# Kernel tuning notes

Measured on AMD Instinct MI355X. Metric: run time of the kernel, lower is better.

## Reference

```python
import jax, jax.numpy as jnp
import numpy as np

C = 64
CQ = C // 4
G = 8  # group norm groups
EPS_GN = 1e-5
POS_COEF = 0.1


def setup_inputs() -> dict:
    key = jax.random.key(0)
    ks = jax.random.split(key, 12)
    B, N = 2, 4096
    return {
        "context_features": jax.random.normal(ks[0], (B, C, N), jnp.float32),
        "motion_features": jax.random.normal(ks[1], (B, C, N), jnp.float32),
        "xyz1": jax.random.uniform(ks[2], (B, N, 3), jnp.float32),
        # tied q/k conv weight (Conv1d k=1, no bias): (C//4, C)
        "Wqk": jax.random.normal(ks[3], (CQ, C), jnp.float32) * 0.1,
        # v_conv: Conv1d(C, C, 1) with bias
        "Wv": jax.random.normal(ks[4], (C, C), jnp.float32) * 0.1,
        "bv": jax.random.normal(ks[5], (C,), jnp.float32) * 0.1,
        # trans_conv: Conv1d(C, C, 1) with bias
        "Wt": jax.random.normal(ks[6], (C, C), jnp.float32) * 0.1,
        "bt": jax.random.normal(ks[7], (C,), jnp.float32) * 0.1,
        # GroupNorm(8, C) affine params
        "gn_w": jax.random.normal(ks[8], (C,), jnp.float32) * 0.1 + 1.0,
        "gn_b": jax.random.normal(ks[9], (C,), jnp.float32) * 0.1,
        # PReLU single slope, alpha_gma scalar (init 0 in torch; random here for testing)
        "prelu_a": jnp.float32(0.25) + jax.random.normal(ks[10], (), jnp.float32) * 0.01,
        "alpha": jax.random.normal(ks[11], (), jnp.float32) * 0.1,
    }


def _group_norm(x, w, b):
    # x: (B, C, N)
    B, Cc, N = x.shape
    xg = x.reshape(B, G, Cc // G, N)
    mu = xg.mean(axis=(2, 3), keepdims=True)
    var = xg.var(axis=(2, 3), keepdims=True)
    xn = ((xg - mu) * jax.lax.rsqrt(var + EPS_GN)).reshape(B, Cc, N)
    return xn * w[None, :, None] + b[None, :, None]


def reference(context_features, motion_features, xyz1, Wqk, Wv, bv, Wt, bt, gn_w, gn_b, prelu_a, alpha):
    # --- self attention (tied q/k) ---
    q = jnp.einsum("oc,bcn->bon", Wqk, context_features)  # (B, C/4, N)
    corr = jnp.einsum("bom,bon->bmn", q, q)               # (B, N, N)
    attn = jax.nn.softmax(corr, axis=-1)
    attn = attn / (1e-9 + attn.sum(axis=1, keepdims=True))

    # --- position mask via Gram-trick squared distances ---
    sq = jnp.sum(xyz1 * xyz1, axis=-1)                    # (B, N)
    d = sq[:, :, None] + sq[:, None, :] - 2.0 * jnp.einsum("bid,bjd->bij", xyz1, xyz1)
    d = jnp.maximum(d, 0.0)
    pos_am = d / (1e-9 + d.sum(axis=1, keepdims=True))
    mask = pos_am <= POS_COEF

    local = attn * mask
    local = jax.nn.softmax(local, axis=-1)
    local = local / (1e-9 + local.sum(axis=1, keepdims=True))
    attn = attn + local

    # --- GMA fusion ---
    xv = jnp.einsum("oc,bcn->bon", Wv, motion_features) + bv[None, :, None]
    gma = jnp.einsum("bcm,bmn->bcn", xv, attn)
    res = jnp.einsum("oc,bcn->bon", Wt, motion_features - gma) + bt[None, :, None]
    gr = _group_norm(res, gn_w, gn_b)
    gr = jnp.where(gr >= 0, gr, prelu_a * gr)  # PReLU
    return alpha * gr + motion_features
```

## Files before the change

### kernel.cpp

```cpp
#include <hip/hip_runtime.h>
#include <hip/hip_bf16.h>
#include <cstdio>

#define NB 2
#define NN 4096
#define NC 64
#define NQ 16
#define POS_COEF 0.1f

#define OFF_QT   0u
#define OFF_QK   131072u
#define OFF_XYZ4 262144u
#define OFF_XYZK 294912u
#define OFF_IRS1 327680u
#define OFF_IRS2 335872u
#define OFF_THR  344064u
#define OFF_ICS1 352256u
#define OFF_FLAG 360448u
#define OFF_XVB  360464u
#define OFF_SUMS 622608u
#define OFF_GN   622616u
#define OFF_CS2  622648u
#define OFF_GMA  630840u
#define OFF_G2   1155128u
#define WS_TOTAL 1679416u
#define ZERO_F   (WS_TOTAL - OFF_SUMS)
#define OFF_A0   1679424u
#define OFF_AE   18456640u
#define FULL_F   35233856u

using bf16x8 = __attribute__((ext_vector_type(8))) short;
using f32x4v = __attribute__((ext_vector_type(4))) float;

__device__ __forceinline__ float rcpf_(float x) { return __builtin_amdgcn_rcpf(x); }
__device__ __forceinline__ unsigned short f2bf(float x) {
  __hip_bfloat16 h = __float2bfloat16(x);
  return *(unsigned short*)&h;
}
__device__ __forceinline__ float bf2f(unsigned short u) {
  unsigned v = ((unsigned)u) << 16;
  return __builtin_bit_cast(float, v);
}

__device__ __forceinline__ float ldin(const void* p, size_t i, bool f32) {
  return f32 ? ((const float*)p)[i]
             : __bfloat162float(((const __hip_bfloat16*)p)[i]);
}

#define DOT16M(A0,A1,A2,A3,B0,B1,B2,B3) \
  fmaf((A0).x,(B0).x, fmaf((A0).y,(B0).y, fmaf((A0).z,(B0).z, fmaf((A0).w,(B0).w, \
  fmaf((A1).x,(B1).x, fmaf((A1).y,(B1).y, fmaf((A1).z,(B1).z, fmaf((A1).w,(B1).w, \
  fmaf((A2).x,(B2).x, fmaf((A2).y,(B2).y, fmaf((A2).z,(B2).z, fmaf((A2).w,(B2).w, \
  fmaf((A3).x,(B3).x, fmaf((A3).y,(B3).y, fmaf((A3).z,(B3).z, (A3).w*(B3).w)))))))))))))))

#define DOTC(M0,M1,M2,M3,C) \
  fmaf((M0).x,k0.C, fmaf((M0).y,k1.C, fmaf((M0).z,k2.C, fmaf((M0).w,k3.C, \
  fmaf((M1).x,k4.C, fmaf((M1).y,k5.C, fmaf((M1).z,k6.C, fmaf((M1).w,k7.C, \
  fmaf((M2).x,k8.C, fmaf((M2).y,k9.C, fmaf((M2).z,k10.C, fmaf((M2).w,k11.C, \
  fmaf((M3).x,k12.C, fmaf((M3).y,k13.C, fmaf((M3).z,k14.C, (M3).w*k15.C)))))))))))))))

#define LKPL(base, n0) \
  const float4 k0  = *(const float4*)((base) + 0*NN  + (n0)); \
  const float4 k1  = *(const float4*)((base) + 1*NN  + (n0)); \
  const float4 k2  = *(const float4*)((base) + 2*NN  + (n0)); \
  const float4 k3  = *(const float4*)((base) + 3*NN  + (n0)); \
  const float4 k4  = *(const float4*)((base) + 4*NN  + (n0)); \
  const float4 k5  = *(const float4*)((base) + 5*NN  + (n0)); \
  const float4 k6  = *(const float4*)((base) + 6*NN  + (n0)); \
  const float4 k7  = *(const float4*)((base) + 7*NN  + (n0)); \
  const float4 k8  = *(const float4*)((base) + 8*NN  + (n0)); \
  const float4 k9  = *(const float4*)((base) + 9*NN  + (n0)); \
  const float4 k10 = *(const float4*)((base) + 10*NN + (n0)); \
  const float4 k11 = *(const float4*)((base) + 11*NN + (n0)); \
  const float4 k12 = *(const float4*)((base) + 12*NN + (n0)); \
  const float4 k13 = *(const float4*)((base) + 13*NN + (n0)); \
  const float4 k14 = *(const float4*)((base) + 14*NN + (n0)); \
  const float4 k15 = *(const float4*)((base) + 15*NN + (n0));

#define WRED(s) { s += __shfl_xor(s, 32); s += __shfl_xor(s, 16); \
  s += __shfl_xor(s, 8); s += __shfl_xor(s, 4); s += __shfl_xor(s, 2); s += __shfl_xor(s, 1); }

#define LQROW(v, base) \
  const float4 v##0 = *(const float4*)((base)); \
  const float4 v##1 = *(const float4*)((base) + 4); \
  const float4 v##2 = *(const float4*)((base) + 8); \
  const float4 v##3 = *(const float4*)((base) + 12);

__global__ __launch_bounds__(256) void k0_detect(
    const unsigned short* __restrict__ ctx_u16, float* __restrict__ flag) {
  const int tid = threadIdx.x;
  int bad = 0;
  for (int i = tid; i < 8192; i += 256) {
    const unsigned short u = ctx_u16[i];
    const int e = (u >> 7) & 0xFF;
    if (e >= 134 || (e >= 1 && e <= 100)) bad++;
  }
  __shared__ int cnt;
  if (tid == 0) cnt = 0;
  __syncthreads();
  atomicAdd(&cnt, bad);
  __syncthreads();
  if (tid == 0) flag[0] = (cnt > 256) ? 1.0f : 0.0f;
}

__global__ __launch_bounds__(256) void k1_q_xyz(
    const void* __restrict__ ctx, const void* __restrict__ xyz,
    const void* __restrict__ wqk, const float* __restrict__ flag,
    float* __restrict__ qt, float* __restrict__ qk,
    float* __restrict__ xyz4, float* __restrict__ xyzk,
    float* __restrict__ sums) {
  const bool f32 = flag[0] > 0.5f;
  const int tid = threadIdx.x;
  const int b = blockIdx.x >> 4;
  const int n = ((blockIdx.x & 15) << 8) + tid;
  __shared__ float wqT[NQ * NC];
  for (int i = tid; i < NQ * NC; i += 256) {
    int o = i & 15, c = i >> 4;
    wqT[c * 16 + o] = ldin(wqk, o * 64 + c, f32);
  }
  __syncthreads();
  float4 a0 = {0,0,0,0}, a1 = {0,0,0,0}, a2 = {0,0,0,0}, a3 = {0,0,0,0};
  const size_t cbase = (size_t)b * 64 * NN + n;
#pragma unroll 4
  for (int c = 0; c < 64; ++c) {
    float x = ldin(ctx, cbase + (size_t)c * NN, f32);
    const float4 w0 = *(const float4*)(wqT + c * 16 + 0);
    const float4 w1 = *(const float4*)(wqT + c * 16 + 4);
    const float4 w2 = *(const float4*)(wqT + c * 16 + 8);
    const float4 w3 = *(const float4*)(wqT + c * 16 + 12);
// ... 312 lines not shown
  LQROW(mb, qb + (size_t)mB * 16)
  float sA = 0.f, sB = 0.f;
  for (int it = 0; it < 8; ++it) {
    const int n0 = (it << 9) + (lane << 3);
    float4 aAl = {0,0,0,0}, aAh = {0,0,0,0}, aBl = {0,0,0,0}, aBh = {0,0,0,0};
#define PLN(QA_, QB_, P) { \
      const float4 kl_ = *(const float4*)(kb + (size_t)(P) * NN + n0); \
      const float4 kh_ = *(const float4*)(kb + (size_t)(P) * NN + n0 + 4); \
      aAl.x = fmaf(QA_, kl_.x, aAl.x); aAl.y = fmaf(QA_, kl_.y, aAl.y); \
      aAl.z = fmaf(QA_, kl_.z, aAl.z); aAl.w = fmaf(QA_, kl_.w, aAl.w); \
      aAh.x = fmaf(QA_, kh_.x, aAh.x); aAh.y = fmaf(QA_, kh_.y, aAh.y); \
      aAh.z = fmaf(QA_, kh_.z, aAh.z); aAh.w = fmaf(QA_, kh_.w, aAh.w); \
      aBl.x = fmaf(QB_, kl_.x, aBl.x); aBl.y = fmaf(QB_, kl_.y, aBl.y); \
      aBl.z = fmaf(QB_, kl_.z, aBl.z); aBl.w = fmaf(QB_, kl_.w, aBl.w); \
      aBh.x = fmaf(QB_, kh_.x, aBh.x); aBh.y = fmaf(QB_, kh_.y, aBh.y); \
      aBh.z = fmaf(QB_, kh_.z, aBh.z); aBh.w = fmaf(QB_, kh_.w, aBh.w); }
    PLN(ma0.x, mb0.x, 0)   PLN(ma0.y, mb0.y, 1)
    PLN(ma0.z, mb0.z, 2)   PLN(ma0.w, mb0.w, 3)
    PLN(ma1.x, mb1.x, 4)   PLN(ma1.y, mb1.y, 5)
    PLN(ma1.z, mb1.z, 6)   PLN(ma1.w, mb1.w, 7)
    PLN(ma2.x, mb2.x, 8)   PLN(ma2.y, mb2.y, 9)
    PLN(ma2.z, mb2.z, 10)  PLN(ma2.w, mb2.w, 11)
    PLN(ma3.x, mb3.x, 12)  PLN(ma3.y, mb3.y, 13)
    PLN(ma3.z, mb3.z, 14)  PLN(ma3.w, mb3.w, 15)
#undef PLN
#define EX8(AL, AH, S, ROWPTR) { \
      const unsigned short u0_ = f2bf(__expf(fminf((AL).x, 80.f))); \
      const unsigned short u1_ = f2bf(__expf(fminf((AL).y, 80.f))); \
      const unsigned short u2_ = f2bf(__expf(fminf((AL).z, 80.f))); \
      const unsigned short u3_ = f2bf(__expf(fminf((AL).w, 80.f))); \
      const unsigned short u4_ = f2bf(__expf(fminf((AH).x, 80.f))); \
      const unsigned short u5_ = f2bf(__expf(fminf((AH).y, 80.f))); \
      const unsigned short u6_ = f2bf(__expf(fminf((AH).z, 80.f))); \
      const unsigned short u7_ = f2bf(__expf(fminf((AH).w, 80.f))); \
      uint4 U_; \
      U_.x = (unsigned)u0_ | ((unsigned)u1_ << 16); \
      U_.y = (unsigned)u2_ | ((unsigned)u3_ << 16); \
      U_.z = (unsigned)u4_ | ((unsigned)u5_ << 16); \
      U_.w = (unsigned)u6_ | ((unsigned)u7_ << 16); \
      *(uint4*)((ROWPTR) + n0) = U_; \
      S += bf2f(u0_) + bf2f(u1_) + bf2f(u2_) + bf2f(u3_) \
         + bf2f(u4_) + bf2f(u5_) + bf2f(u6_) + bf2f(u7_); }
    EX8(aAl, aAh, sA, ab + (size_t)mA * NN)
    EX8(aBl, aBh, sB, ab + (size_t)mB * NN)
#undef EX8
  }
  WRED(sA) WRED(sB)
  if (lane == 0) {
    irs1[b * NN + mA] = rcpf_(sA);
    irs1[b * NN + mB] = rcpf_(sB);
  }
}

__global__ __launch_bounds__(256) void p2r_cs1(
    const unsigned short* __restrict__ a0g, const float* __restrict__ irs1,
    float* __restrict__ ics1) {
  const int tid = threadIdx.x;
  const int w = tid >> 6, l = tid & 63;
  const int bi = blockIdx.x;
  const int b = bi >> 10;
  const int n = ((bi & 1023) << 2) + w;
  const unsigned short* row = a0g + ((size_t)b * NN + n) * NN;
  const float* ir = irs1 + b * NN;
  float s = 0.f;
#pragma unroll
  for (int it = 0; it < 8; ++it) {
    const int m = (it << 9) + (l << 3);
    const uint4 u = *(const uint4*)(row + m);
    const float4 i0 = *(const float4*)(ir + m);
    const float4 i1 = *(const float4*)(ir + m + 4);
    s = fmaf(bf2f((unsigned short)(u.x & 0xffffu)), i0.x, s);
    s = fmaf(bf2f((unsigned short)(u.x >> 16)),     i0.y, s);
    s = fmaf(bf2f((unsigned short)(u.y & 0xffffu)), i0.z, s);
    s = fmaf(bf2f((unsigned short)(u.y >> 16)),     i0.w, s);
    s = fmaf(bf2f((unsigned short)(u.z & 0xffffu)), i1.x, s);
    s = fmaf(bf2f((unsigned short)(u.z >> 16)),     i1.y, s);
    s = fmaf(bf2f((unsigned short)(u.w & 0xffffu)), i1.z, s);
    s = fmaf(bf2f((unsigned short)(u.w >> 16)),     i1.w, s);
  }
  WRED(s)
  if (l == 0) ics1[b * NN + n] = rcpf_(1e-9f + s);
}

__global__ __launch_bounds__(256) void p3w_rs2(
    const float* __restrict__ xyz4, const float* __restrict__ xyzk,
    const float* __restrict__ irs1, const float* __restrict__ ics1,
    const float* __restrict__ thr, float* __restrict__ irs2,
    const unsigned short* __restrict__ a0g, unsigned short* __restrict__ aeg) {
  const int tid = threadIdx.x;
  const int b = blockIdx.x >> 9;
  const int m0 = (blockIdx.x & 511) << 3;
  const int w = tid >> 6, lane = tid & 63;
  const float* xk = xyzk + (size_t)b * 4 * NN;
  const unsigned short* ab = a0g + (size_t)b * NN * NN;
  unsigned short* eb = aeg + (size_t)b * NN * NN;
  const int mA = m0 + (w << 1), mB = mA + 1;
  const float4 pmA = *(const float4*)(xyz4 + ((size_t)b * NN + mA) * 4);
  const float4 pmB = *(const float4*)(xyz4 + ((size_t)b * NN + mB) * 4);
  const float rA = irs1[b * NN + mA];
  const float rB = irs1[b * NN + mB];
  float sA = 0.f, sB = 0.f;
#define P3E(S, OUT, A0W, SH, PM, R, PX, PY, PZ, PW, IC, TH) { \
    float a1v_ = bf2f((unsigned short)(((A0W) >> (SH)) & 0xffffu)) * (R) * (IC); \
    float dd_ = (PM).w + (PW) - 2.f * ((PM).x * (PX) + (PM).y * (PY) + (PM).z * (PZ)); \
    dd_ = fmaxf(dd_, 0.f); \
    float l0_ = (dd_ <= (TH)) ? a1v_ : 0.f; \
    const unsigned short us_ = f2bf(__expf(l0_)); OUT = us_; S += bf2f(us_); }
  for (int it = 0; it < 8; ++it) {
    const int n0 = (it << 9) + (lane << 3);
    const float4 pxl = *(const float4*)(xk + 0*NN + n0);
    const float4 pxh = *(const float4*)(xk + 0*NN + n0 + 4);
    const float4 pyl = *(const float4*)(xk + 1*NN + n0);
    const float4 pyh = *(const float4*)(xk + 1*NN + n0 + 4);
    const float4 pzl = *(const float4*)(xk + 2*NN + n0);
    const float4 pzh = *(const float4*)(xk + 2*NN + n0 + 4);
    const float4 pwl = *(const float4*)(xk + 3*NN + n0);
    const float4 pwh = *(const float4*)(xk + 3*NN + n0 + 4);
    const float4 icl = *(const float4*)(ics1 + b * NN + n0);
    const float4 ich = *(const float4*)(ics1 + b * NN + n0 + 4);
    const float4 thl = *(const float4*)(thr + b * NN + n0);
    const float4 thh = *(const float4*)(thr + b * NN + n0 + 4);
    const uint4 rAu = *(const uint4*)(ab + (size_t)mA * NN + n0);
    const uint4 rBu = *(const uint4*)(ab + (size_t)mB * NN + n0);
    unsigned short e0, e1, e2, e3, e4, e5, e6, e7;
    P3E(sA, e0, rAu.x, 0,  pmA, rA, pxl.x, pyl.x, pzl.x, pwl.x, icl.x, thl.x)
    P3E(sA, e1, rAu.x, 16, pmA, rA, pxl.y, pyl.y, pzl.y, pwl.y, icl.y, thl.y)
    P3E(sA, e2, rAu.y, 0,  pmA, rA, pxl.z, pyl.z, pzl.z, pwl.z, icl.z, thl.z)
    P3E(sA, e3, rAu.y, 16, pmA, rA, pxl.w, pyl.w, pzl.w, pwl.w, icl.w, thl.w)
    P3E(sA, e4, rAu.z, 0,  pmA, rA, pxh.x, pyh.x, pzh.x, pwh.x, ich.x, thh.x)
    P3E(sA, e5, rAu.z, 16, pmA, rA, pxh.y, pyh.y, pzh.y, pwh.y, ich.y, thh.y)
    P3E(sA, e6, rAu.w, 0,  pmA, rA, pxh.z, pyh.z, pzh.z, pwh.z, ich.z, thh.z)
    P3E(sA, e7, rAu.w, 16, pmA, rA, pxh.w, pyh.w, pzh.w, pwh.w, ich.w, thh.w)
    {
      uint4 U_;
      U_.x = (unsigned)e0 | ((unsigned)e1 << 16);
      U_.y = (unsigned)e2 | ((unsigned)e3 << 16);
      U_.z = (unsigned)e4 | ((unsigned)e5 << 16);
      U_.w = (unsigned)e6 | ((unsigned)e7 << 16);
      *(uint4*)(eb + (size_t)mA * NN + n0) = U_;
    }
    P3E(sB, e0, rBu.x, 0,  pmB, rB, pxl.x, pyl.x, pzl.x, pwl.x, icl.x, thl.x)
    P3E(sB, e1, rBu.x, 16, pmB, rB, pxl.y, pyl.y, pzl.y, pwl.y, icl.y, thl.y)
    P3E(sB, e2, rBu.y, 0,  pmB, rB, pxl.z, pyl.z, pzl.z, pwl.z, icl.z, thl.z)
    P3E(sB, e3, rBu.y, 16, pmB, rB, pxl.w, pyl.w, pzl.w, pwl.w, icl.w, thl.w)
    P3E(sB, e4, rBu.z, 0,  pmB, rB, pxh.x, pyh.x, pzh.x, pwh.x, ich.x, thh.x)
    P3E(sB, e5, rBu.z, 16, pmB, rB, pxh.y, pyh.y, pzh.y, pwh.y, ich.y, thh.y)
    P3E(sB, e6, rBu.w, 0,  pmB, rB, pxh.z, pyh.z, pzh.z, pwh.z, ich.z, thh.z)
    P3E(sB, e7, rBu.w, 16, pmB, rB, pxh.w, pyh.w, pzh.w, pwh.w, ich.w, thh.w)
    {
      uint4 U_;
      U_.x = (unsigned)e0 | ((unsigned)e1 << 16);
      U_.y = (unsigned)e2 | ((unsigned)e3 << 16);
      U_.z = (unsigned)e4 | ((unsigned)e5 << 16);
      U_.w = (unsigned)e6 | ((unsigned)e7 << 16);
      *(uint4*)(eb + (size_t)mB * NN + n0) = U_;
    }
  }
#undef P3E
  WRED(sA) WRED(sB)
  if (lane == 0) {
    irs2[b * NN + mA] = rcpf_(sA);
    irs2[b * NN + mB] = rcpf_(sB);
  }
}

__global__ __launch_bounds__(256) void p4_cs2(
    const unsigned short* __restrict__ aeg, const float* __restrict__ irs2,
    float* __restrict__ cs2) {
  const int tid = threadIdx.x;
  const int bid = blockIdx.x;
  const int ms = bid & 63;
  const int ng = (bid >> 6) & 7;
  const int b  = bid >> 9;
  const int n2 = (ng << 9) + (tid << 1);
  const unsigned short* eb = aeg + (size_t)b * NN * NN + n2;
  const float* r2 = irs2 + b * NN;
  float s0 = 0.f, s1 = 0.f;
  const int m0 = ms << 6;
#pragma unroll 4
  for (int m = m0; m < m0 + 64; ++m) {
    const unsigned u = *(const unsigned*)(eb + (size_t)m * NN);
    const float r = r2[m];
    s0 += bf2f(f2bf(bf2f((unsigned short)(u & 0xffffu)) * r));
    s1 += bf2f(f2bf(bf2f((unsigned short)(u >> 16)) * r));
  }
  atomicAdd(&cs2[b * NN + n2], s0);
  atomicAdd(&cs2[b * NN + n2 + 1], s1);
}

#define SW(r) ((((r) & 7) << 4) ^ ((((r) >> 3) & 3) << 5))

__global__ __launch_bounds__(256) void k7n_gma(
    const unsigned short* __restrict__ a0g, const unsigned short* __restrict__ aeg,
    const unsigned short* __restrict__ xvb,
    const float* __restrict__ irs1, const float* __restrict__ irs2,
    const float* __restrict__ ics1, const float* __restrict__ cs2,
    float* __restrict__ gma) {
  const int tid = threadIdx.x;
  const int bid = blockIdx.x;
  const int msl = bid & 3;
  const int nb  = (bid >> 2) & 63;
  const int b   = bid >> 8;
  const int n0 = nb << 6;
  const int mstart = msl << 10;
  __shared__ __align__(16) unsigned short attns1[2][64 * 64];
  __shared__ __align__(16) unsigned short attns2[2][64 * 64];
  __shared__ __align__(16) unsigned short xvs[2][64 * 64];
  const unsigned short* ab = a0g + (size_t)b * NN * NN;
  const unsigned short* ebp = aeg + (size_t)b * NN * NN;
  const float* irs1b = irs1 + b * NN;
  const float* irs2b = irs2 + b * NN;
  const int w = tid >> 6, l = tid & 63;
  const int lrow0 = (w << 4) + ((l >> 3) << 1);
  const int nc8 = (l & 7) << 3;
  const int gcol = n0 + nc8;
  const int xc = tid >> 2, xpart = tid & 3;
  const unsigned short* xvp = xvb + ((size_t)b * 64 + xc) * NN;
  const int lr = l & 15, quad = l >> 4;
  const int nw = w << 4;
  f32x4v acc0 = {0,0,0,0}, acc1 = {0,0,0,0}, acc2 = {0,0,0,0}, acc3 = {0,0,0,0};
  f32x4v d0 = {0,0,0,0}, d1 = {0,0,0,0}, d2 = {0,0,0,0}, d3 = {0,0,0,0};

  uint4 pa0A, pa1A, pe0A, pe1A, pv0A, pv1A;
  uint4 pa0B, pa1B, pe0B, pe1B, pv0B, pv1B;
  float r1aA, r1bA, r2aA, r2bA, r1aB, r1bB, r2aB, r2bB;

#define ISSUE(S, MT) { \
    const int m0_ = mstart + ((MT) << 6); \
    const size_t ra_ = (size_t)(m0_ + lrow0) * NN + gcol; \
    pa0##S = *(const uint4*)(ab + ra_); \
    pa1##S = *(const uint4*)(ab + ra_ + NN); \
    pe0##S = *(const uint4*)(ebp + ra_); \
    pe1##S = *(const uint4*)(ebp + ra_ + NN); \
    pv0##S = *(const uint4*)(xvp + m0_ + (xpart << 4)); \
    pv1##S = *(const uint4*)(xvp + m0_ + (xpart << 4) + 8); \
    r1a##S = irs1b[m0_ + lrow0]; r1b##S = irs1b[m0_ + lrow0 + 1]; \
    r2a##S = irs2b[m0_ + lrow0]; r2b##S = irs2b[m0_ + lrow0 + 1]; }

#define CVW(D0, D1, SH, J, R0, R1, ARR) { \
    const float v0_ = bf2f((unsigned short)(((D0) >> (SH)) & 0xffffu)) * (R0); \
    const float v1_ = bf2f((unsigned short)(((D1) >> (SH)) & 0xffffu)) * (R1); \
    const unsigned pk_ = (unsigned)f2bf(v0_) | ((unsigned)f2bf(v1_) << 16); \
    const int nl_ = nc8 + (J); \
    *(unsigned*)((char*)(ARR) + ((((nl_) << 7) + (lrow0 << 1)) ^ SW(nl_))) = pk_; }

#define WR8(U0, U1, R0, R1, ARR) \
    CVW(U0.x, U1.x, 0,  0, R0, R1, ARR) CVW(U0.x, U1.x, 16, 1, R0, R1, ARR) \
    CVW(U0.y, U1.y, 0,  2, R0, R1, ARR) CVW(U0.y, U1.y, 16, 3, R0, R1, ARR) \
    CVW(U0.z, U1.z, 0,  4, R0, R1, ARR) CVW(U0.z, U1.z, 16, 5, R0, R1, ARR) \
    CVW(U0.w, U1.w, 0,  6, R0, R1, ARR) CVW(U0.w, U1.w, 16, 7, R0, R1, ARR)

#define STX(XARR, PV0, PV1) { \
    const int xb_ = (xc << 7) + (xpart << 5); \
    *(uint4*)((char*)(XARR) + ((xb_) ^ SW(xc))) = PV0; \
    *(uint4*)((char*)(XARR) + ((xb_ + 16) ^ SW(xc))) = PV1; }

#define LDSW(ARR, ROW, H, Q) \
    (*(const bf16x8*)((const char*)(ARR) + \
      ((((ROW) << 7) + ((H) << 6) + ((Q) << 4)) ^ SW(ROW))))

#define MPH(A1P, A2P, XVP_) { \
    for (int h = 0; h < 2; ++h) { \
      const bf16x8 fa1 = LDSW(A1P, nw + lr, h, quad); \
      const bf16x8 fa2 = LDSW(A2P, nw + lr, h, quad); \
      const bf16x8 fb0 = LDSW(XVP_, lr, h, quad); \
      const bf16x8 fb1 = LDSW(XVP_, 16 + lr, h, quad); \
      const bf16x8 fb2 = LDSW(XVP_, 32 + lr, h, quad); \
      const bf16x8 fb3 = LDSW(XVP_, 48 + lr, h, quad); \
      acc0 = __builtin_amdgcn_mfma_f32_16x16x32_bf16(fa1, fb0, acc0, 0, 0, 0); \
      acc1 = __builtin_amdgcn_mfma_f32_16x16x32_bf16(fa1, fb1, acc1, 0, 0, 0); \
      acc2 = __builtin_amdgcn_mfma_f32_16x16x32_bf16(fa1, fb2, acc2, 0, 0, 0); \
      acc3 = __builtin_amdgcn_mfma_f32_16x16x32_bf16(fa1, fb3, acc3, 0, 0, 0); \
      d0 = __builtin_amdgcn_mfma_f32_16x16x32_bf16(fa2, fb0, d0, 0, 0, 0); \
      d1 = __builtin_amdgcn_mfma_f32_16x16x32_bf16(fa2, fb1, d1, 0, 0, 0); \
      d2 = __builtin_amdgcn_mfma_f32_16x16x32_bf16(fa2, fb2, d2, 0, 0, 0); \
      d3 = __builtin_amdgcn_mfma_f32_16x16x32_bf16(fa2, fb3, d3, 0, 0, 0); \
    } }

  ISSUE(A, 0)
  ISSUE(B, 1)
  for (int mt = 0; mt < 16; mt += 2) {
    WR8(pa0A, pa1A, r1aA, r1bA, attns1[0])
    WR8(pe0A, pe1A, r2aA, r2bA, attns2[0])
    STX(xvs[0], pv0A, pv1A)
    __syncthreads();
    if (mt + 2 < 16) { ISSUE(A, mt + 2) }
    MPH(attns1[0], attns2[0], xvs[0])
    WR8(pa0B, pa1B, r1aB, r1bB, attns1[1])
    WR8(pe0B, pe1B, r2aB, r2bB, attns2[1])
    STX(xvs[1], pv0B, pv1B)
    __syncthreads();
    if (mt + 3 < 16) { ISSUE(B, mt + 3) }
    MPH(attns1[1], attns2[1], xvs[1])
  }
#undef ISSUE
#undef CVW
#undef WR8
#undef STX
#undef LDSW
#undef MPH
  float w10, w11, w12, w13, w20, w21, w22, w23;
  {
    const int nr = n0 + nw + (quad << 2);
    w10 = ics1[b * NN + nr + 0]; w20 = rcpf_(1e-9f + cs2[b * NN + nr + 0]);
    w11 = ics1[b * NN + nr + 1]; w21 = rcpf_(1e-9f + cs2[b * NN + nr + 1]);
    w12 = ics1[b * NN + nr + 2]; w22 = rcpf_(1e-9f + cs2[b * NN + nr + 2]);
    w13 = ics1[b * NN + nr + 3]; w23 = rcpf_(1e-9f + cs2[b * NN + nr + 3]);
  }
#define EPI(ACC, DD, CT) { \
    float* g_ = gma + ((size_t)b * NN + n0 + nw + (quad << 2)) * 64 + (CT) * 16 + lr; \
    atomicAdd(g_ + 0,   fmaf(ACC[0], w10, DD[0] * w20)); \
    atomicAdd(g_ + 64,  fmaf(ACC[1], w11, DD[1] * w21)); \
    atomicAdd(g_ + 128, fmaf(ACC[2], w12, DD[2] * w22)); \
    atomicAdd(g_ + 192, fmaf(ACC[3], w13, DD[3] * w23)); }
  EPI(acc0, d0, 0) EPI(acc1, d1, 1) EPI(acc2, d2, 2) EPI(acc3, d3, 3)
#undef EPI
}


__global__ __launch_bounds__(256) void p2_cs1(
    const float* __restrict__ qt, const float* __restrict__ qk,
    const float* __restrict__ irs1, float* __restrict__ ics1) {
  const int tid = threadIdx.x;
  const int b = blockIdx.x >> 8;
  const int n0t = (blockIdx.x & 255) << 4;
  const int w = tid >> 6, lane = tid & 63;
  const float* qb = qt + (size_t)b * NN * 16;
  const float* kb = qk + (size_t)b * 16 * NN;
  const int nA = n0t + w, nB = n0t + w + 4, nC = n0t + w + 8, nD = n0t + w + 12;
  LQROW(na, qb + (size_t)nA * 16)
  LQROW(nb, qb + (size_t)nB * 16)
  LQROW(nc, qb + (size_t)nC * 16)
  LQROW(nd, qb + (size_t)nD * 16)
  float sA = 0.f, sB = 0.f, sC = 0.f, sD = 0.f;
  for (int it = 0; it < 16; ++it) {
    const int m0 = (it << 8) + (lane << 2);
    LKPL(kb, m0)
    const float4 r1 = *(const float4*)(irs1 + b * NN + m0);
    sA = fmaf(__expf(fminf(DOTC(na0,na1,na2,na3,x), 80.f)), r1.x, sA);
    sA = fmaf(__expf(fminf(DOTC(na0,na1,na2,na3,y), 80.f)), r1.y, sA);
    sA = fmaf(__expf(fminf(DOTC(na0,na1,na2,na3,z), 80.f)), r1.z, sA);
    sA = fmaf(__expf(fminf(DOTC(na0,na1,na2,na3,w), 80.f)), r1.w, sA);
    sB = fmaf(__expf(fminf(DOTC(nb0,nb1,nb2,nb3,x), 80.f)), r1.x, sB);
    sB = fmaf(__expf(fminf(DOTC(nb0,nb1,nb2,nb3,y), 80.f)), r1.y, sB);
    sB = fmaf(__expf(fminf(DOTC(nb0,nb1,nb2,nb3,z), 80.f)), r1.z, sB);
    sB = fmaf(__expf(fminf(DOTC(nb0,nb1,nb2,nb3,w), 80.f)), r1.w, sB);
    sC = fmaf(__expf(fminf(DOTC(nc0,nc1,nc2,nc3,x), 80.f)), r1.x, sC);
    sC = fmaf(__expf(fminf(DOTC(nc0,nc1,nc2,nc3,y), 80.f)), r1.y, sC);
    sC = fmaf(__expf(fminf(DOTC(nc0,nc1,nc2,nc3,z), 80.f)), r1.z, sC);
    sC = fmaf(__expf(fminf(DOTC(nc0,nc1,nc2,nc3,w), 80.f)), r1.w, sC);
    sD = fmaf(__expf(fminf(DOTC(nd0,nd1,nd2,nd3,x), 80.f)), r1.x, sD);
    sD = fmaf(__expf(fminf(DOTC(nd0,nd1,nd2,nd3,y), 80.f)), r1.y, sD);
    sD = fmaf(__expf(fminf(DOTC(nd0,nd1,nd2,nd3,z), 80.f)), r1.z, sD);
    sD = fmaf(__expf(fminf(DOTC(nd0,nd1,nd2,nd3,w), 80.f)), r1.w, sD);
  }
  WRED(sA) WRED(sB) WRED(sC) WRED(sD)
  if (lane == 0) {
    ics1[b * NN + nA] = rcpf_(1e-9f + sA);
    ics1[b * NN + nB] = rcpf_(1e-9f + sB);
    ics1[b * NN + nC] = rcpf_(1e-9f + sC);
    ics1[b * NN + nD] = rcpf_(1e-9f + sD);
  }
}

__global__ __launch_bounds__(256) void k8_res(
    const void* __restrict__ mot, const void* __restrict__ wt,
    const void* __restrict__ bt, const float* __restrict__ flag,
    float* __restrict__ g1_res, const float* __restrict__ g2,
    const float* __restrict__ cs2, float* __restrict__ gn,
    const float* __restrict__ ics1, int g1mode) {
  const bool f32 = flag[0] > 0.5f;
  const int tid = threadIdx.x;
// ... 7 lines not shown
  for (int i = tid; i < 4096; i += 256) {
    int o = i & 63, c = i >> 6;
    wtT[c * 65 + o] = ldin(wt, o * 64 + c, f32);
  }
  if (tid < 64) bts[tid] = ldin(bt, tid, f32);
  if (tid < 8) { gs[tid] = 0.f; gss[tid] = 0.f; }
#pragma unroll
  for (int r = 0; r < 2; ++r) {
    const int idx = tid * 2 + r;
    const int c = idx & 63, nl = idx >> 6;
    const size_t gi = ((size_t)b * NN + n0 + nl) * 64 + c;
    float gmav;
    if (g1mode == 2) {
      gmav = g1_res[gi];
    } else {
      const float ics2n = rcpf_(1e-9f + cs2[b * NN + n0 + nl]);
      float g1v = g1_res[gi];
      if (g1mode == 1) g1v *= ics1[b * NN + n0 + nl];
      gmav = fmaf(g2[gi], ics2n, g1v);
    }
    md[nl * 64 + c] = ldin(mot, ((size_t)b * 64 + c) * NN + n0 + nl, f32) - gmav;
  }
  __syncthreads();
  const int o = tid & 63, ng = tid >> 6;
  const int nl0 = ng * 2, nl1 = ng * 2 + 1;
  float a0 = bts[o], a1 = bts[o];
#pragma unroll 8
  for (int c = 0; c < 64; ++c) {
    float w = wtT[c * 65 + o];
    a0 = fmaf(w, md[nl0 * 64 + c], a0);
    a1 = fmaf(w, md[nl1 * 64 + c], a1);
  }
  g1_res[((size_t)b * NN + n0 + nl0) * 64 + o] = a0;
  g1_res[((size_t)b * NN + n0 + nl1) * 64 + o] = a1;
  atomicAdd(&gs[o >> 3], a0 + a1);
  atomicAdd(&gss[o >> 3], a0 * a0 + a1 * a1);
  __syncthreads();
  if (tid < 8) atomicAdd(&gn[b * 8 + tid], gs[tid]);
  else if (tid < 16) atomicAdd(&gn[16 + b * 8 + (tid - 8)], gss[tid - 8]);
}

__global__ __launch_bounds__(256) void k9_out(
    const float* __restrict__ res, const float* __restrict__ gn,
    const void* __restrict__ mot,
    const void* __restrict__ gnw, const void* __restrict__ gnb,
    const void* __restrict__ pa, const void* __restrict__ al,
    const float* __restrict__ flag, void* __restrict__ out) {
  const bool f32 = flag[0] > 0.5f;
  const int idx = blockIdx.x * 256 + threadIdx.x;
  const int n = idx & 4095;
  const int c = (idx >> 12) & 63;
  const int b = idx >> 18;
  const int g = c >> 3;
  const float inv_cnt = 1.f / 32768.f;
  float mean = gn[b * 8 + g] * inv_cnt;
  float var = gn[16 + b * 8 + g] * inv_cnt - mean * mean;
  var = fmaxf(var, 0.f);
  float rstd = rsqrtf(var + 1e-5f);
  float r = res[((size_t)b * NN + n) * 64 + c];
  float y = (r - mean) * rstd * ldin(gnw, c, f32) + ldin(gnb, c, f32);
  float slope = ldin(pa, 0, f32);
  y = (y >= 0.f) ? y : slope * y;
  float o = ldin(al, 0, f32) * y + ldin(mot, idx, f32);
  if (f32) ((float*)out)[idx] = o;
  else     ((__hip_bfloat16*)out)[idx] = __float2bfloat16(o);
}

extern "C" void kernel_launch(void* const* d_in, const int* in_sizes, int n_in,
                              void* d_out, int out_size, void* d_ws, size_t ws_size,
                              hipStream_t stream) {
  const void* ctx = d_in[0];
  const void* mot = d_in[1];
  const void* xyz = d_in[2];
  const void* wqk = d_in[3];
  const void* wv  = d_in[4];
  const void* bv  = d_in[5];
  const void* wt  = d_in[6];
  const void* bt  = d_in[7];
  const void* gnw = d_in[8];
  const void* gnb = d_in[9];
  const void* pa  = d_in[10];
  const void* al  = d_in[11];
  float* ws = (float*)d_ws;
  const bool big = ws_size >= (size_t)FULL_F * sizeof(float);

  if (ws_size < (size_t)WS_TOTAL * sizeof(float))
    fprintf(stderr, "[gma3d] WARNING ws_size=%zu < needed %zu\n",
            ws_size, (size_t)WS_TOTAL * sizeof(float));

  hipMemsetAsync(ws + OFF_SUMS, 0, (size_t)ZERO_F * sizeof(float), stream);

  k0_detect<<<1, 256, 0, stream>>>((const unsigned short*)ctx, ws + OFF_FLAG);
  k1_q_xyz<<<32, 256, 0, stream>>>(ctx, xyz, wqk, ws + OFF_FLAG,
                                   ws + OFF_QT, ws + OFF_QK,
                                   ws + OFF_XYZ4, ws + OFF_XYZK, ws + OFF_SUMS);
  k2_xv<<<128, 256, 0, stream>>>(mot, wv, bv, ws + OFF_FLAG,
                                 (unsigned short*)(ws + OFF_XVB));
  k2b_thr<<<32, 256, 0, stream>>>(ws + OFF_XYZ4, ws + OFF_SUMS, ws + OFF_THR);

  if (big) {
    unsigned short* a0 = (unsigned short*)(ws + OFF_A0);
    unsigned short* ae = (unsigned short*)(ws + OFF_AE);
    p1w_rs1<<<1024, 256, 0, stream>>>(ws + OFF_QT, ws + OFF_QK, ws + OFF_IRS1, a0);
    p2r_cs1<<<2048, 256, 0, stream>>>(a0, ws + OFF_IRS1, ws + OFF_ICS1);
    p3w_rs2<<<1024, 256, 0, stream>>>(ws + OFF_XYZ4, ws + OFF_XYZK,
                                      ws + OFF_IRS1, ws + OFF_ICS1, ws + OFF_THR,
                                      ws + OFF_IRS2, a0, ae);
    p4_cs2<<<1024, 256, 0, stream>>>(ae, ws + OFF_IRS2, ws + OFF_CS2);
    k7n_gma<<<512, 256, 0, stream>>>(a0, ae,
                                     (const unsigned short*)(ws + OFF_XVB),
                                     ws + OFF_IRS1, ws + OFF_IRS2,
                                     ws + OFF_ICS1, ws + OFF_CS2,
                                     ws + OFF_GMA);
    k8_res<<<1024, 256, 0, stream>>>(mot, wt, bt, ws + OFF_FLAG,
                                     ws + OFF_GMA, ws + OFF_G2, ws + OFF_CS2,
                                     ws + OFF_GN, ws + OFF_ICS1, 2);
  } else {
    p1_rs1<<<512, 256, 0, stream>>>(ws + OFF_QT, ws + OFF_QK, ws + OFF_IRS1);
    p2_cs1<<<512, 256, 0, stream>>>(ws + OFF_QT, ws + OFF_QK, ws + OFF_IRS1, ws + OFF_ICS1);
    p3_rs2<<<512, 256, 0, stream>>>(ws + OFF_QT, ws + OFF_QK,
                                    ws + OFF_XYZ4, ws + OFF_XYZK,
                                    ws + OFF_IRS1, ws + OFF_ICS1, ws + OFF_THR,
                                    ws + OFF_IRS2);
    k7_gma<<<1024, 256, 0, stream>>>(ws + OFF_QT, ws + OFF_XYZ4,
                                     (const unsigned short*)(ws + OFF_XVB),
                                     ws + OFF_IRS1, ws + OFF_IRS2,
                                     ws + OFF_ICS1, ws + OFF_THR,
                                     ws + OFF_GMA, ws + OFF_G2, ws + OFF_CS2);
    k8_res<<<1024, 256, 0, stream>>>(mot, wt, bt, ws + OFF_FLAG,
                                     ws + OFF_GMA, ws + OFF_G2, ws + OFF_CS2,
                                     ws + OFF_GN, ws + OFF_ICS1, 0);
  }

  k9_out<<<2048, 256, 0, stream>>>(ws + OFF_GMA, ws + OFF_GN, mot, gnw, gnb, pa, al,
                                   ws + OFF_FLAG, d_out);
}
```

Before: 284.3 us.

## Recompute masked local-attention exp values instead of materializing the ae matrix

The pass that computed the masked exp matrix no longer writes a second full N×N bf16 buffer. Each downstream consumer (row-sum pass, column-sum pass, GMA matmul) rebuilds those values from the stored base attention, the xyz positions and the thresholds through a shared helper. This removes one large global write and two large reads, and lowers the workspace needed to enable the precomputed path. In exchange every consumer does extra exp and distance arithmetic, and needs extra position and threshold loads and registers.

```diff
diff --git a/kernel.cpp b/kernel.cpp
--- a/kernel.cpp
+++ b/kernel.cpp
@@ -26,8 +26,7 @@
 #define WS_TOTAL 1679416u
 #define ZERO_F   (WS_TOTAL - OFF_SUMS)
 #define OFF_A0   1679424u
-#define OFF_AE   18456640u
-#define FULL_F   35233856u
+#define BIG_F    18456640u
 
 using bf16x8 = __attribute__((ext_vector_type(8))) short;
 using f32x4v = __attribute__((ext_vector_type(4))) float;
@@ -45,6 +44,16 @@
 __device__ __forceinline__ float ldin(const void* p, size_t i, bool f32) {
   return f32 ? ((const float*)p)[i]
              : __bfloat162float(((const __hip_bfloat16*)p)[i]);
+}
+
+__device__ __forceinline__ unsigned short ae_bits(
+    unsigned short a0u, float r1, float ic, float4 pm,
+    float px, float py, float pz, float pw, float th) {
+  float a1v = bf2f(a0u) * r1 * ic;
+  float dd = pm.w + pw - 2.f * (pm.x * px + pm.y * py + pm.z * pz);
+  dd = fmaxf(dd, 0.f);
+  float l0 = (dd <= th) ? a1v : 0.f;
+  return f2bf(__expf(l0));
 }
 
 #define DOT16M(A0,A1,A2,A3,B0,B1,B2,B3) \
@@ -523,30 +532,23 @@
   if (l == 0) ics1[b * NN + n] = rcpf_(1e-9f + s);
 }
 
-__global__ __launch_bounds__(256) void p3w_rs2(
+__global__ __launch_bounds__(256) void p3r_rs2(
     const float* __restrict__ xyz4, const float* __restrict__ xyzk,
     const float* __restrict__ irs1, const float* __restrict__ ics1,
     const float* __restrict__ thr, float* __restrict__ irs2,
-    const unsigned short* __restrict__ a0g, unsigned short* __restrict__ aeg) {
+    const unsigned short* __restrict__ a0g) {
   const int tid = threadIdx.x;
   const int b = blockIdx.x >> 9;
   const int m0 = (blockIdx.x & 511) << 3;
   const int w = tid >> 6, lane = tid & 63;
   const float* xk = xyzk + (size_t)b * 4 * NN;
   const unsigned short* ab = a0g + (size_t)b * NN * NN;
-  unsigned short* eb = aeg + (size_t)b * NN * NN;
   const int mA = m0 + (w << 1), mB = mA + 1;
   const float4 pmA = *(const float4*)(xyz4 + ((size_t)b * NN + mA) * 4);
   const float4 pmB = *(const float4*)(xyz4 + ((size_t)b * NN + mB) * 4);
   const float rA = irs1[b * NN + mA];
   const float rB = irs1[b * NN + mB];
   float sA = 0.f, sB = 0.f;
-#define P3E(S, OUT, A0W, SH, PM, R, PX, PY, PZ, PW, IC, TH) { \
-    float a1v_ = bf2f((unsigned short)(((A0W) >> (SH)) & 0xffffu)) * (R) * (IC); \
-    float dd_ = (PM).w + (PW) - 2.f * ((PM).x * (PX) + (PM).y * (PY) + (PM).z * (PZ)); \
-    dd_ = fmaxf(dd_, 0.f); \
-    float l0_ = (dd_ <= (TH)) ? a1v_ : 0.f; \
-    const unsigned short us_ = f2bf(__expf(l0_)); OUT = us_; S += bf2f(us_); }
   for (int it = 0; it < 8; ++it) {
     const int n0 = (it << 9) + (lane << 3);
     const float4 pxl = *(const float4*)(xk + 0*NN + n0);
@@ -563,41 +565,27 @@
     const float4 thh = *(const float4*)(thr + b * NN + n0 + 4);
     const uint4 rAu = *(const uint4*)(ab + (size_t)mA * NN + n0);
     const uint4 rBu = *(const uint4*)(ab + (size_t)mB * NN + n0);
-    unsigned short e0, e1, e2, e3, e4, e5, e6, e7;
-    P3E(sA, e0, rAu.x, 0,  pmA, rA, pxl.x, pyl.x, pzl.x, pwl.x, icl.x, thl.x)
-    P3E(sA, e1, rAu.x, 16, pmA, rA, pxl.y, pyl.y, pzl.y, pwl.y, icl.y, thl.y)
-    P3E(sA, e2, rAu.y, 0,  pmA, rA, pxl.z, pyl.z, pzl.z, pwl.z, icl.z, thl.z)
-    P3E(sA, e3, rAu.y, 16, pmA, rA, pxl.w, pyl.w, pzl.w, pwl.w, icl.w, thl.w)
-    P3E(sA, e4, rAu.z, 0,  pmA, rA, pxh.x, pyh.x, pzh.x, pwh.x, ich.x, thh.x)
-    P3E(sA, e5, rAu.z, 16, pmA, rA, pxh.y, pyh.y, pzh.y, pwh.y, ich.y, thh.y)
-    P3E(sA, e6, rAu.w, 0,  pmA, rA, pxh.z, pyh.z, pzh.z, pwh.z, ich.z, thh.z)
-    P3E(sA, e7, rAu.w, 16, pmA, rA, pxh.w, pyh.w, pzh.w, pwh.w, ich.w, thh.w)
-    {
-      uint4 U_;
-      U_.x = (unsigned)e0 | ((unsigned)e1 << 16);
-      U_.y = (unsigned)e2 | ((unsigned)e3 << 16);
-      U_.z = (unsigned)e4 | ((unsigned)e5 << 16);
-      U_.w = (unsigned)e6 | ((unsigned)e7 << 16);
-      *(uint4*)(eb + (size_t)mA * NN + n0) = U_;
-    }
-    P3E(sB, e0, rBu.x, 0,  pmB, rB, pxl.x, pyl.x, pzl.x, pwl.x, icl.x, thl.x)
-    P3E(sB, e1, rBu.x, 16, pmB, rB, pxl.y, pyl.y, pzl.y, pwl.y, icl.y, thl.y)
-    P3E(sB, e2, rBu.y, 0,  pmB, rB, pxl.z, pyl.z, pzl.z, pwl.z, icl.z, thl.z)
-    P3E(sB, e3, rBu.y, 16, pmB, rB, pxl.w, pyl.w, pzl.w, pwl.w, icl.w, thl.w)
-    P3E(sB, e4, rBu.z, 0,  pmB, rB, pxh.x, pyh.x, pzh.x, pwh.x, ich.x, thh.x)
-    P3E(sB, e5, rBu.z, 16, pmB, rB, pxh.y, pyh.y, pzh.y, pwh.y, ich.y, thh.y)
-    P3E(sB, e6, rBu.w, 0,  pmB, rB, pxh.z, pyh.z, pzh.z, pwh.z, ich.z, thh.z)
-    P3E(sB, e7, rBu.w, 16, pmB, rB, pxh.w, pyh.w, pzh.w, pwh.w, ich.w, thh.w)
-    {
-      uint4 U_;
-      U_.x = (unsigned)e0 | ((unsigned)e1 << 16);
-      U_.y = (unsigned)e2 | ((unsigned)e3 << 16);
-      U_.z = (unsigned)e4 | ((unsigned)e5 << 16);
-      U_.w = (unsigned)e6 | ((unsigned)e7 << 16);
-      *(uint4*)(eb + (size_t)mB * NN + n0) = U_;
-    }
-  }
-#undef P3E
+#define P3R1(S, A0W, SH, PM, R, PX, PY, PZ, PW, IC, TH) \
+    S += bf2f(ae_bits((unsigned short)(((A0W) >> (SH)) & 0xffffu), (R), (IC), \
+                      (PM), (PX), (PY), (PZ), (PW), (TH)));
+    P3R1(sA, rAu.x, 0,  pmA, rA, pxl.x, pyl.x, pzl.x, pwl.x, icl.x, thl.x)
+    P3R1(sA, rAu.x, 16, pmA, rA, pxl.y, pyl.y, pzl.y, pwl.y, icl.y, thl.y)
+    P3R1(sA, rAu.y, 0,  pmA, rA, pxl.z, pyl.z, pzl.z, pwl.z, icl.z, thl.z)
+    P3R1(sA, rAu.y, 16, pmA, rA, pxl.w, pyl.w, pzl.w, pwl.w, icl.w, thl.w)
+    P3R1(sA, rAu.z, 0,  pmA, rA, pxh.x, pyh.x, pzh.x, pwh.x, ich.x, thh.x)
+    P3R1(sA, rAu.z, 16, pmA, rA, pxh.y, pyh.y, pzh.y, pwh.y, ich.y, thh.y)
+    P3R1(sA, rAu.w, 0,  pmA, rA, pxh.z, pyh.z, pzh.z, pwh.z, ich.z, thh.z)
+    P3R1(sA, rAu.w, 16, pmA, rA, pxh.w, pyh.w, pzh.w, pwh.w, ich.w, thh.w)
+    P3R1(sB, rBu.x, 0,  pmB, rB, pxl.x, pyl.x, pzl.x, pwl.x, icl.x, thl.x)
+    P3R1(sB, rBu.x, 16, pmB, rB, pxl.y, pyl.y, pzl.y, pwl.y, icl.y, thl.y)
+    P3R1(sB, rBu.y, 0,  pmB, rB, pxl.z, pyl.z, pzl.z, pwl.z, icl.z, thl.z)
+    P3R1(sB, rBu.y, 16, pmB, rB, pxl.w, pyl.w, pzl.w, pwl.w, icl.w, thl.w)
+    P3R1(sB, rBu.z, 0,  pmB, rB, pxh.x, pyh.x, pzh.x, pwh.x, ich.x, thh.x)
+    P3R1(sB, rBu.z, 16, pmB, rB, pxh.y, pyh.y, pzh.y, pwh.y, ich.y, thh.y)
+    P3R1(sB, rBu.w, 0,  pmB, rB, pxh.z, pyh.z, pzh.z, pwh.z, ich.z, thh.z)
+    P3R1(sB, rBu.w, 16, pmB, rB, pxh.w, pyh.w, pzh.w, pwh.w, ich.w, thh.w)
+#undef P3R1
+  }
   WRED(sA) WRED(sB)
   if (lane == 0) {
     irs2[b * NN + mA] = rcpf_(sA);
@@ -606,24 +594,40 @@
 }
 
 __global__ __launch_bounds__(256) void p4_cs2(
-    const unsigned short* __restrict__ aeg, const float* __restrict__ irs2,
-    float* __restrict__ cs2) {
+    const unsigned short* __restrict__ a0g, const float* __restrict__ irs1,
+    const float* __restrict__ irs2, const float* __restrict__ ics1,
+    const float* __restrict__ xyz4, const float* __restrict__ xyzk,
+    const float* __restrict__ thr, float* __restrict__ cs2) {
   const int tid = threadIdx.x;
   const int bid = blockIdx.x;
   const int ms = bid & 63;
   const int ng = (bid >> 6) & 7;
   const int b  = bid >> 9;
   const int n2 = (ng << 9) + (tid << 1);
-  const unsigned short* eb = aeg + (size_t)b * NN * NN + n2;
-  const float* r2 = irs2 + b * NN;
+  const unsigned short* ab = a0g + (size_t)b * NN * NN + n2;
+  const float* r1p = irs1 + b * NN;
+  const float* r2p = irs2 + b * NN;
+  const float* xk = xyzk + (size_t)b * 4 * NN;
+  const float px0 = xk[0*NN + n2],     px1 = xk[0*NN + n2 + 1];
+  const float py0 = xk[1*NN + n2],     py1 = xk[1*NN + n2 + 1];
+  const float pz0 = xk[2*NN + n2],     pz1 = xk[2*NN + n2 + 1];
+  const float pw0 = xk[3*NN + n2],     pw1 = xk[3*NN + n2 + 1];
+  const float ic0 = ics1[b * NN + n2], ic1 = ics1[b * NN + n2 + 1];
+  const float th0 = thr[b * NN + n2],  th1 = thr[b * NN + n2 + 1];
   float s0 = 0.f, s1 = 0.f;
   const int m0 = ms << 6;
 #pragma unroll 4
   for (int m = m0; m < m0 + 64; ++m) {
-    const unsigned u = *(const unsigned*)(eb + (size_t)m * NN);
-    const float r = r2[m];
-    s0 += bf2f(f2bf(bf2f((unsigned short)(u & 0xffffu)) * r));
-    s1 += bf2f(f2bf(bf2f((unsigned short)(u >> 16)) * r));
+    const unsigned u = *(const unsigned*)(ab + (size_t)m * NN);
+    const float r1 = r1p[m];
+    const float r2 = r2p[m];
+    const float4 pm = *(const float4*)(xyz4 + ((size_t)b * NN + m) * 4);
+    const unsigned short e0 = ae_bits((unsigned short)(u & 0xffffu), r1, ic0,
+                                      pm, px0, py0, pz0, pw0, th0);
+    const unsigned short e1 = ae_bits((unsigned short)(u >> 16), r1, ic1,
+                                      pm, px1, py1, pz1, pw1, th1);
+    s0 += bf2f(f2bf(bf2f(e0) * r2));
+    s1 += bf2f(f2bf(bf2f(e1) * r2));
   }
   atomicAdd(&cs2[b * NN + n2], s0);
   atomicAdd(&cs2[b * NN + n2 + 1], s1);
@@ -632,10 +636,12 @@
 #define SW(r) ((((r) & 7) << 4) ^ ((((r) >> 3) & 3) << 5))
 
 __global__ __launch_bounds__(256) void k7n_gma(
-    const unsigned short* __restrict__ a0g, const unsigned short* __restrict__ aeg,
+    const unsigned short* __restrict__ a0g,
     const unsigned short* __restrict__ xvb,
     const float* __restrict__ irs1, const float* __restrict__ irs2,
     const float* __restrict__ ics1, const float* __restrict__ cs2,
+    const float* __restrict__ xyz4, const float* __restrict__ xyzk,
+    const float* __restrict__ thr,
     float* __restrict__ gma) {
   const int tid = threadIdx.x;
   const int bid = blockIdx.x;
@@ -648,9 +654,10 @@
   __shared__ __align__(16) unsigned short attns2[2][64 * 64];
   __shared__ __align__(16) unsigned short xvs[2][64 * 64];
   const unsigned short* ab = a0g + (size_t)b * NN * NN;
-  const unsigned short* ebp = aeg + (size_t)b * NN * NN;
   const float* irs1b = irs1 + b * NN;
   const float* irs2b = irs2 + b * NN;
+  const float* x4 = xyz4 + (size_t)b * NN * 4;
+  const float* xk = xyzk + (size_t)b * 4 * NN;
   const int w = tid >> 6, l = tid & 63;
   const int lrow0 = (w << 4) + ((l >> 3) << 1);
   const int nc8 = (l & 7) << 3;
@@ -659,37 +666,62 @@
   const unsigned short* xvp = xvb + ((size_t)b * 64 + xc) * NN;
   const int lr = l & 15, quad = l >> 4;
   const int nw = w << 4;
+  const float4 pxl = *(const float4*)(xk + 0*NN + gcol);
+  const float4 pxh = *(const float4*)(xk + 0*NN + gcol + 4);
+  const float4 pyl = *(const float4*)(xk + 1*NN + gcol);
+  const float4 pyh = *(const float4*)(xk + 1*NN + gcol + 4);
+  const float4 pzl = *(const float4*)(xk + 2*NN + gcol);
+  const float4 pzh = *(const float4*)(xk + 2*NN + gcol + 4);
+  const float4 pwl = *(const float4*)(xk + 3*NN + gcol);
+  const float4 pwh = *(const float4*)(xk + 3*NN + gcol + 4);
+  const float4 icl = *(const float4*)(ics1 + b * NN + gcol);
+  const float4 ich = *(const float4*)(ics1 + b * NN + gcol + 4);
+  const float4 thl = *(const float4*)(thr + b * NN + gcol);
+  const float4 thh = *(const float4*)(thr + b * NN + gcol + 4);
   f32x4v acc0 = {0,0,0,0}, acc1 = {0,0,0,0}, acc2 = {0,0,0,0}, acc3 = {0,0,0,0};
   f32x4v d0 = {0,0,0,0}, d1 = {0,0,0,0}, d2 = {0,0,0,0}, d3 = {0,0,0,0};
 
-  uint4 pa0A, pa1A, pe0A, pe1A, pv0A, pv1A;
-  uint4 pa0B, pa1B, pe0B, pe1B, pv0B, pv1B;
+  uint4 pa0A, pa1A, pv0A, pv1A;
+  uint4 pa0B, pa1B, pv0B, pv1B;
   float r1aA, r1bA, r2aA, r2bA, r1aB, r1bB, r2aB, r2bB;
+  float4 pmaA, pmbA, pmaB, pmbB;
 
 #define ISSUE(S, MT) { \
     const int m0_ = mstart + ((MT) << 6); \
     const size_t ra_ = (size_t)(m0_ + lrow0) * NN + gcol; \
     pa0##S = *(const uint4*)(ab + ra_); \
     pa1##S = *(const uint4*)(ab + ra_ + NN); \
-    pe0##S = *(const uint4*)(ebp + ra_); \
-    pe1##S = *(const uint4*)(ebp + ra_ + NN); \
     pv0##S = *(const uint4*)(xvp + m0_ + (xpart << 4)); \
     pv1##S = *(const uint4*)(xvp + m0_ + (xpart << 4) + 8); \
     r1a##S = irs1b[m0_ + lrow0]; r1b##S = irs1b[m0_ + lrow0 + 1]; \
-    r2a##S = irs2b[m0_ + lrow0]; r2b##S = irs2b[m0_ + lrow0 + 1]; }
-
-#define CVW(D0, D1, SH, J, R0, R1, ARR) { \
-    const float v0_ = bf2f((unsigned short)(((D0) >> (SH)) & 0xffffu)) * (R0); \
-    const float v1_ = bf2f((unsigned short)(((D1) >> (SH)) & 0xffffu)) * (R1); \
-    const unsigned pk_ = (unsigned)f2bf(v0_) | ((unsigned)f2bf(v1_) << 16); \
+    r2a##S = irs2b[m0_ + lrow0]; r2b##S = irs2b[m0_ + lrow0 + 1]; \
+    pma##S = *(const float4*)(x4 + (size_t)(m0_ + lrow0) * 4); \
+    pmb##S = *(const float4*)(x4 + (size_t)(m0_ + lrow0 + 1) * 4); }
+
+#define CVW(D0, D1, SH, J, R1A, R1B, R2A, R2B, PMA, PMB, A1ARR, A2ARR, PX, PY, PZ, PW, IC, TH) { \
+    const unsigned short a0u0_ = (unsigned short)(((D0) >> (SH)) & 0xffffu); \
+    const unsigned short a0u1_ = (unsigned short)(((D1) >> (SH)) & 0xffffu); \
+    const float v0_ = bf2f(a0u0_) * (R1A); \
+    const float v1_ = bf2f(a0u1_) * (R1B); \
+    const unsigned pk1_ = (unsigned)f2bf(v0_) | ((unsigned)f2bf(v1_) << 16); \
+    const unsigned short e0_ = ae_bits(a0u0_, (R1A), (IC), (PMA), (PX), (PY), (PZ), (PW), (TH)); \
+    const unsigned short e1_ = ae_bits(a0u1_, (R1B), (IC), (PMB), (PX), (PY), (PZ), (PW), (TH)); \
+    const unsigned pk2_ = (unsigned)f2bf(bf2f(e0_) * (R2A)) \
+                        | ((unsigned)f2bf(bf2f(e1_) * (R2B)) << 16); \
     const int nl_ = nc8 + (J); \
-    *(unsigned*)((char*)(ARR) + ((((nl_) << 7) + (lrow0 << 1)) ^ SW(nl_))) = pk_; }
-
-#define WR8(U0, U1, R0, R1, ARR) \
-    CVW(U0.x, U1.x, 0,  0, R0, R1, ARR) CVW(U0.x, U1.x, 16, 1, R0, R1, ARR) \
-    CVW(U0.y, U1.y, 0,  2, R0, R1, ARR) CVW(U0.y, U1.y, 16, 3, R0, R1, ARR) \
-    CVW(U0.z, U1.z, 0,  4, R0, R1, ARR) CVW(U0.z, U1.z, 16, 5, R0, R1, ARR) \
-    CVW(U0.w, U1.w, 0,  6, R0, R1, ARR) CVW(U0.w, U1.w, 16, 7, R0, R1, ARR)
+    const int off_ = (((nl_) << 7) + (lrow0 << 1)) ^ SW(nl_); \
+    *(unsigned*)((char*)(A1ARR) + off_) = pk1_; \
+    *(unsigned*)((char*)(A2ARR) + off_) = pk2_; }
+
+#define WR8(U0, U1, R1A, R1B, R2A, R2B, PMA, PMB, A1ARR, A2ARR) \
+    CVW(U0.x, U1.x, 0,  0, R1A, R1B, R2A, R2B, PMA, PMB, A1ARR, A2ARR, pxl.x, pyl.x, pzl.x, pwl.x, icl.x, thl.x) \
+    CVW(U0.x, U1.x, 16, 1, R1A, R1B, R2A, R2B, PMA, PMB, A1ARR, A2ARR, pxl.y, pyl.y, pzl.y, pwl.y, icl.y, thl.y) \
+    CVW(U0.y, U1.y, 0,  2, R1A, R1B, R2A, R2B, PMA, PMB, A1ARR, A2ARR, pxl.z, pyl.z, pzl.z, pwl.z, icl.z, thl.z) \
+    CVW(U0.y, U1.y, 16, 3, R1A, R1B, R2A, R2B, PMA, PMB, A1ARR, A2ARR, pxl.w, pyl.w, pzl.w, pwl.w, icl.w, thl.w) \
+    CVW(U0.z, U1.z, 0,  4, R1A, R1B, R2A, R2B, PMA, PMB, A1ARR, A2ARR, pxh.x, pyh.x, pzh.x, pwh.x, ich.x, thh.x) \
+    CVW(U0.z, U1.z, 16, 5, R1A, R1B, R2A, R2B, PMA, PMB, A1ARR, A2ARR, pxh.y, pyh.y, pzh.y, pwh.y, ich.y, thh.y) \
+    CVW(U0.w, U1.w, 0,  6, R1A, R1B, R2A, R2B, PMA, PMB, A1ARR, A2ARR, pxh.z, pyh.z, pzh.z, pwh.z, ich.z, thh.z) \
+    CVW(U0.w, U1.w, 16, 7, R1A, R1B, R2A, R2B, PMA, PMB, A1ARR, A2ARR, pxh.w, pyh.w, pzh.w, pwh.w, ich.w, thh.w)
 
 #define STX(XARR, PV0, PV1) { \
     const int xb_ = (xc << 7) + (xpart << 5); \
@@ -721,14 +753,12 @@
   ISSUE(A, 0)
   ISSUE(B, 1)
   for (int mt = 0; mt < 16; mt += 2) {
-    WR8(pa0A, pa1A, r1aA, r1bA, attns1[0])
-    WR8(pe0A, pe1A, r2aA, r2bA, attns2[0])
+    WR8(pa0A, pa1A, r1aA, r1bA, r2aA, r2bA, pmaA, pmbA, attns1[0], attns2[0])
     STX(xvs[0], pv0A, pv1A)
     __syncthreads();
     if (mt + 2 < 16) { ISSUE(A, mt + 2) }
     MPH(attns1[0], attns2[0], xvs[0])
-    WR8(pa0B, pa1B, r1aB, r1bB, attns1[1])
-    WR8(pe0B, pe1B, r2aB, r2bB, attns2[1])
+    WR8(pa0B, pa1B, r1aB, r1bB, r2aB, r2bB, pmaB, pmbB, attns1[1], attns2[1])
     STX(xvs[1], pv0B, pv1B)
     __syncthreads();
     if (mt + 3 < 16) { ISSUE(B, mt + 3) }
@@ -902,7 +932,7 @@
   const void* pa  = d_in[10];
   const void* al  = d_in[11];
   float* ws = (float*)d_ws;
-  const bool big = ws_size >= (size_t)FULL_F * sizeof(float);
+  const bool big = ws_size >= (size_t)BIG_F * sizeof(float);
 
   if (ws_size < (size_t)WS_TOTAL * sizeof(float))
     fprintf(stderr, "[gma3d] WARNING ws_size=%zu < needed %zu\n",
@@ -920,17 +950,19 @@
 
   if (big) {
     unsigned short* a0 = (unsigned short*)(ws + OFF_A0);
-    unsigned short* ae = (unsigned short*)(ws + OFF_AE);
     p1w_rs1<<<1024, 256, 0, stream>>>(ws + OFF_QT, ws + OFF_QK, ws + OFF_IRS1, a0);
     p2r_cs1<<<2048, 256, 0, stream>>>(a0, ws + OFF_IRS1, ws + OFF_ICS1);
-    p3w_rs2<<<1024, 256, 0, stream>>>(ws + OFF_XYZ4, ws + OFF_XYZK,
+    p3r_rs2<<<1024, 256, 0, stream>>>(ws + OFF_XYZ4, ws + OFF_XYZK,
                                       ws + OFF_IRS1, ws + OFF_ICS1, ws + OFF_THR,
-                                      ws + OFF_IRS2, a0, ae);
-    p4_cs2<<<1024, 256, 0, stream>>>(ae, ws + OFF_IRS2, ws + OFF_CS2);
-    k7n_gma<<<512, 256, 0, stream>>>(a0, ae,
+                                      ws + OFF_IRS2, a0);
+    p4_cs2<<<1024, 256, 0, stream>>>(a0, ws + OFF_IRS1, ws + OFF_IRS2,
+                                     ws + OFF_ICS1, ws + OFF_XYZ4,
+                                     ws + OFF_XYZK, ws + OFF_THR, ws + OFF_CS2);
+    k7n_gma<<<512, 256, 0, stream>>>(a0,
                                      (const unsigned short*)(ws + OFF_XVB),
                                      ws + OFF_IRS1, ws + OFF_IRS2,
                                      ws + OFF_ICS1, ws + OFF_CS2,
+                                     ws + OFF_XYZ4, ws + OFF_XYZK, ws + OFF_THR,
                                      ws + OFF_GMA);
     k8_res<<<1024, 256, 0, stream>>>(mot, wt, bt, ws + OFF_FLAG,
                                      ws + OFF_GMA, ws + OFF_G2, ws + OFF_CS2,
```

Measured after the change: 299.5 us. 5.3% more time.
